# Kernel optimization log

Measured on AMD Instinct MI355X. Metric: run time of the kernel, lower is better.

## Reference

```python
import jax, jax.numpy as jnp
import numpy as np

S, B, D = 1024, 32, 1024

def setup_inputs() -> dict:
    key = jax.random.key(0)
    k1, k2, k3, k4, k5 = jax.random.split(key, 5)
    x = jax.random.normal(k1, (S, B, D), dtype=jnp.float32)
    layer_input = jax.random.normal(k2, (S, B, D), dtype=jnp.float32)
    position_embedding = jax.random.normal(k3, (S, B, D), dtype=jnp.float32)
    # pad indicator == 1 (True); random pads, ~half the positions
    encoder_mask = jax.random.randint(k4, (B, S), 0, 2).astype(bool)
    W = jax.random.normal(k5, (D, 1), dtype=jnp.float32) * (1.0 / np.sqrt(D))
    b = jnp.zeros((1,), dtype=jnp.float32)
    return {"x": x, "layer_input": layer_input,
            "position_embedding": position_embedding,
            "encoder_mask": encoder_mask, "W": W, "b": b}

def reference(x, layer_input, position_embedding, encoder_mask, W, b):
    s, bsz, d = x.shape
    valid = (~encoder_mask).astype(x.dtype)            # (B, S)
    sentence_length = valid.sum(axis=-1)               # (B,)
    langtok_index = s - sentence_length                # (B,)
    # predicted soft position in [0, sentence_length]
    pred = jax.nn.sigmoid(x @ W + b)[..., 0]           # (S, B)
    pred = pred * sentence_length[None, :]             # (S, B)
    # absolute positions shifted by language-token offset
    all_pos = jnp.arange(s, dtype=x.dtype)[:, None] - langtok_index[None, :]  # (S, B)
    # distances[i, b, j] = pred[i, b] - all_pos[j, b]
    dist = pred[:, :, None] - all_pos.T[None, :, :]    # (S, B, S)
    prob = 1.0 / (dist * dist + 0.001)                 # reciprocal squared distance
    prob = prob * valid[None, :, :]                    # zero out pads along j
    prob = prob / prob.sum(axis=-1, keepdims=True)     # normalize over source positions
    # weighted sum of position embeddings: (S,B,S) x (S,B,D) -> (S,B,D)
    out = jnp.einsum('ibj,jbd->ibd', prob, position_embedding)
    out = out * valid.T[:, :, None]                    # zero out pad rows
    return out
```

## Files before the change

kernel.cpp:

```cpp
#include <hip/hip_runtime.h>


#define S_ 1024
#define B_ 32
#define D_ 1024

typedef unsigned short us;
typedef __attribute__((ext_vector_type(4))) unsigned short us4;
typedef __attribute__((ext_vector_type(4))) float f4;
typedef __attribute__((ext_vector_type(8))) short short8;

__device__ __forceinline__ float bf2f(us u){
  unsigned v = ((unsigned)u) << 16;
  float f;
  __builtin_memcpy(&f, &v, 4);
  return f;
}
__device__ __forceinline__ us f2bf(float f){
  unsigned v;
  __builtin_memcpy(&v, &f, 4);
  v = v + 0x7fffu + ((v >> 16) & 1u);
  return (us)(v >> 16);
}

__device__ __forceinline__ void gll16(const void* g, void* l){
  __builtin_amdgcn_global_load_lds(
      (const __attribute__((address_space(1))) void*)g,
      (__attribute__((address_space(3))) void*)l,
      16, 0, 0);
}

__global__ __launch_bounds__(256) void prep_k(const unsigned char* __restrict__ mask,
                                              float* __restrict__ valid,
                                              float* __restrict__ slen,
                                              float* __restrict__ ltok)
{
  const int b = blockIdx.x;
  const int t = threadIdx.x;
  __shared__ int flags[5];
  __shared__ int red[256];
  if (t < 5) flags[t] = 0;
  __syncthreads();
  for (int k = 0; k < 32; ++k){
    int p = t * 32 + k;
    unsigned v = mask[p];
    if (v){
      atomicOr(&flags[p & 3], 1);
      if (v > 1u) atomicOr(&flags[4], 1);
    }
  }
  __syncthreads();
  int fmt;
  int any123 = flags[1] | flags[2] | flags[3];
  if (!flags[4]) fmt = any123 ? 0 : 1;
  else           fmt = (flags[0] | flags[1]) ? 2 : 3;

  int cnt = 0;
#pragma unroll
  for (int q = 0; q < 4; ++q){
    int j = t + q * 256;
    size_t idx = (size_t)b * S_ + j;
    unsigned mv;
    if (fmt == 0)      mv = mask[idx];
    else if (fmt == 1) mv = ((const unsigned int*)mask)[idx];
    else if (fmt == 2) mv = ((const unsigned short*)mask)[idx];
    else               mv = ((const unsigned int*)mask)[idx] & 0x7fffffffu;
    valid[idx] = mv ? 0.0f : 1.0f;
    cnt += mv ? 0 : 1;
  }
  red[t] = cnt;
  __syncthreads();
  for (int s = 128; s > 0; s >>= 1){
    if (t < s) red[t] += red[t + s];
    __syncthreads();
  }
  if (t == 0){
    float cn = (float)red[0];
    slen[b] = cn;
    ltok[b] = (float)S_ - cn;
  }
}

__device__ __forceinline__ void rowk_body(int blk, const float* __restrict__ x,
                                          const float* __restrict__ Wp,
                                          const float* __restrict__ bp,
                                          const float* __restrict__ valid,
                                          const float* __restrict__ slen,
                                          const float* __restrict__ ltok,
                                          us* __restrict__ P,
                                          float* __restrict__ rs,
                                          float* __restrict__ c_arr,
                                          bool writeP)
{
  const int wid  = threadIdx.x >> 6;
  const int lane = threadIdx.x & 63;
  const int row  = blk * 4 + wid;
  const int b = row & (B_ - 1);
  const int i = row >> 5;

  const float4* xr = (const float4*)(x + (size_t)row * D_);
  const float4* wr = (const float4*)Wp;
  float acc = 0.f;
#pragma unroll
  for (int q = 0; q < 4; ++q){
    float4 xv = xr[q * 64 + lane];
    float4 wv = wr[q * 64 + lane];
    acc += xv.x * wv.x + xv.y * wv.y + xv.z * wv.z + xv.w * wv.w;
  }
#pragma unroll
  for (int off = 32; off > 0; off >>= 1) acc += __shfl_xor(acc, off);

  float z   = acc + bp[0];
  float sig = 1.f / (1.f + expf(-z));
  float c   = sig * slen[b] + ltok[b];

  const float4* vr = (const float4*)(valid + (size_t)b * S_);
  us4* Pr = (us4*)(P + ((size_t)b * S_ + i) * S_);
  float wsum = 0.f;
#pragma unroll
  for (int q = 0; q < 4; ++q){
    int idx = q * 64 + lane;
    float4 vv = vr[idx];
    float j0 = (float)(idx * 4);
    float d0 = c - j0;
    float d1 = c - (j0 + 1.f);
    float d2 = c - (j0 + 2.f);
    float d3 = c - (j0 + 3.f);
    us p0 = f2bf(vv.x / (d0 * d0 + 1e-3f));
    us p1 = f2bf(vv.y / (d1 * d1 + 1e-3f));
    us p2 = f2bf(vv.z / (d2 * d2 + 1e-3f));
    us p3 = f2bf(vv.w / (d3 * d3 + 1e-3f));
    if (writeP){
      us4 pv; pv.x = p0; pv.y = p1; pv.z = p2; pv.w = p3;
      Pr[idx] = pv;
    }
    wsum += bf2f(p0) + bf2f(p1) + bf2f(p2) + bf2f(p3);
  }
#pragma unroll
  for (int off = 32; off > 0; off >>= 1) wsum += __shfl_xor(wsum, off);

  if (lane == 0){
    float vi = valid[(size_t)b * S_ + i];
    rs[(size_t)b * S_ + i] = (vi != 0.f) ? (vi / wsum) : 0.f;
    c_arr[(size_t)b * S_ + i] = c;
  }
}

__device__ __forceinline__ void transp_body(int j0, int d0, int b,
                                            const float* __restrict__ pe,
                                            us* __restrict__ Etr,
                                            us* tile )
{
  const int t  = threadIdx.x;
  const int rr = t >> 4, cc = t & 15;
#pragma unroll
  for (int q = 0; q < 4; ++q){
    int j = q * 16 + rr;
    float4 v = *(const float4*)(pe + ((size_t)(j0 + j) * B_ + b) * D_ + d0 + cc * 4);
    us4 tv; tv.x = f2bf(v.x); tv.y = f2bf(v.y); tv.z = f2bf(v.z); tv.w = f2bf(v.w);
    *(us4*)&tile[j * 68 + cc * 4] = tv;
  }
  __syncthreads();
#pragma unroll
  for (int q = 0; q < 4; ++q){
    int d = q * 16 + rr;
    us4 v;
    v.x = tile[(cc * 4 + 0) * 68 + d];
    v.y = tile[(cc * 4 + 1) * 68 + d];
    v.z = tile[(cc * 4 + 2) * 68 + d];
    v.w = tile[(cc * 4 + 3) * 68 + d];
    *(us4*)(Etr + ((size_t)b * D_ + d0 + d) * S_ + j0 + cc * 4) = v;
  }
}

__global__ __launch_bounds__(256) void mid_k(const float* __restrict__ x,
                                             const float* __restrict__ Wp,
                                             const float* __restrict__ bp,
                                             const float* __restrict__ valid,
                                             const float* __restrict__ slen,
                                             const float* __restrict__ ltok,
                                             us* __restrict__ P,
                                             float* __restrict__ rs,
                                             float* __restrict__ c_arr,
                                             const float* __restrict__ pe,
                                             us* __restrict__ Etr)
{
  __shared__ us tile[64 * 68];
  const int bid = blockIdx.x;
  if (bid < (S_ * B_ / 4)){
    rowk_body(bid, x, Wp, bp, valid, slen, ltok, P, rs, c_arr, true);
  } else {
    int id2 = bid - (S_ * B_ / 4);
    int jt = id2 & 15;
    int dt = (id2 >> 4) & 15;
    int b  = id2 >> 8;
    transp_body(jt * 64, dt * 64, b, pe, Etr, tile);
  }
}

__global__ __launch_bounds__(256) void gemm_k(const us* __restrict__ P,
                                              const us* __restrict__ Etr,
                                              const float* __restrict__ rs,
                                              float* __restrict__ out)
{
  const int bid  = blockIdx.x;
  const int xcd  = bid & 7;
  const int s    = bid >> 3;
  const int b    = xcd * 4 + (s >> 6);
  const int tile = s & 63;
  const int i0   = (tile >> 3) * 128;
  const int n0   = (tile & 7) * 128;

  const int t = threadIdx.x;
  const int w = t >> 6;
  const int l = t & 63;
  const int wm = w >> 1, wn = w & 1;
  const int ml = l & 15, quad = l >> 4;

  __shared__ __align__(16) us sA[128 * 64];
  __shared__ __align__(16) us sB[128 * 64];

  const us* gA[4]; const us* gB[4];
  us* lA[4]; us* lB[4];
#pragma unroll
  for (int q = 0; q < 4; ++q){
    int p = (w * 4 + q) * 64 + l;
    int r = p >> 3;
    int c = (p & 7) ^ (r & 7);
    gA[q] = P   + ((size_t)b * S_ + (i0 + r)) * S_ + c * 8;
    gB[q] = Etr + ((size_t)b * D_ + (n0 + r)) * S_ + c * 8;
    lA[q] = sA + (w * 4 + q) * 512;
    lB[q] = sB + (w * 4 + q) * 512;
  }

  f4 acc[4][4];
#pragma unroll
  for (int mt = 0; mt < 4; ++mt)
#pragma unroll
    for (int nt = 0; nt < 4; ++nt){
      f4 zf = {0.0f, 0.0f, 0.0f, 0.0f};
      acc[mt][nt] = zf;
    }

  int arow[4], brow[4];
#pragma unroll
  for (int mt = 0; mt < 4; ++mt) arow[mt] = wm * 64 + mt * 16 + ml;
#pragma unroll
  for (int nt = 0; nt < 4; ++nt) brow[nt] = wn * 64 + nt * 16 + ml;

  for (int kt = 0; kt < S_; kt += 64){
    if (kt) __syncthreads();
#pragma unroll
    for (int q = 0; q < 4; ++q) gll16(gA[q] + kt, lA[q]);
#pragma unroll
    for (int q = 0; q < 4; ++q) gll16(gB[q] + kt, lB[q]);
    __syncthreads();
#pragma unroll
    for (int ks = 0; ks < 2; ++ks){
      short8 av[4], bv[4];
      const int cbase = ks * 4 + quad;
#pragma unroll
      for (int mt = 0; mt < 4; ++mt){
        int r = arow[mt];
        av[mt] = *(const short8*)(sA + (r * 8 + (cbase ^ (r & 7))) * 8);
      }
#pragma unroll
      for (int nt = 0; nt < 4; ++nt){
        int r = brow[nt];
        bv[nt] = *(const short8*)(sB + (r * 8 + (cbase ^ (r & 7))) * 8);
      }
#pragma unroll
      for (int mt = 0; mt < 4; ++mt)
#pragma unroll
        for (int nt = 0; nt < 4; ++nt)
          acc[mt][nt] = __builtin_amdgcn_mfma_f32_16x16x32_bf16(av[mt], bv[nt], acc[mt][nt], 0, 0, 0);
    }
  }

  const float* rsb = rs + (size_t)b * S_;
#pragma unroll
  for (int mt = 0; mt < 4; ++mt){
#pragma unroll
    for (int reg = 0; reg < 4; ++reg){
      int i = i0 + wm * 64 + mt * 16 + quad * 4 + reg;
      float rv = rsb[i];
      size_t ob = ((size_t)i * B_ + b) * D_;
#pragma unroll
      for (int nt = 0; nt < 4; ++nt){
        int d = n0 + wn * 64 + nt * 16 + ml;
        out[ob + d] = acc[mt][nt][reg] * rv;
      }
    }
  }
}

__global__ __launch_bounds__(256) void rowk_nb(const float* __restrict__ x,
                                               const float* __restrict__ Wp,
                                               const float* __restrict__ bp,
                                               const float* __restrict__ valid,
                                               const float* __restrict__ slen,
                                               const float* __restrict__ ltok,
                                               float* __restrict__ rs,
                                               float* __restrict__ c_arr)
{
  rowk_body(blockIdx.x, x, Wp, bp, valid, slen, ltok, nullptr, rs, c_arr, false);
}

__global__ __launch_bounds__(256) void slow_out_k(const float* __restrict__ pe,
                                                  const float* __restrict__ valid,
                                                  const float* __restrict__ c_arr,
                                                  const float* __restrict__ rs,
                                                  float* __restrict__ out)
{
  const int bid = blockIdx.x;
  const int b = bid & (B_ - 1);
  const int i = bid >> 5;
  const int t = threadIdx.x;
  __shared__ float sw[S_];
  float c  = c_arr[(size_t)b * S_ + i];
  float rv = rs[(size_t)b * S_ + i];
#pragma unroll
  for (int q = 0; q < 4; ++q){
    int j = t + q * 256;
    float d = c - (float)j;
    sw[j] = valid[(size_t)b * S_ + j] / (d * d + 1e-3f);
  }
  __syncthreads();
  float a0 = 0, a1 = 0, a2 = 0, a3 = 0;
  if (rv != 0.0f){
    for (int j = 0; j < S_; ++j){
      float wj = sw[j];
      const float* row = pe + ((size_t)j * B_ + b) * D_;
      a0 += wj * row[t];
      a1 += wj * row[t + 256];
      a2 += wj * row[t + 512];
      a3 += wj * row[t + 768];
    }
  }
  float* orow = out + ((size_t)i * B_ + b) * D_;
  orow[t]       = a0 * rv;
  orow[t + 256] = a1 * rv;
  orow[t + 512] = a2 * rv;
  orow[t + 768] = a3 * rv;
}

extern "C" void kernel_launch(void* const* d_in, const int* in_sizes, int n_in,
                              void* d_out, int out_size, void* d_ws, size_t ws_size,
                              hipStream_t stream)
{
  (void)in_sizes; (void)n_in; (void)out_size;
  const float* x  = (const float*)d_in[0];
  const float* pe = (const float*)d_in[2];
  const unsigned char* mask = (const unsigned char*)d_in[3];
  const float* Wp = (const float*)d_in[4];
  const float* bp = (const float*)d_in[5];
  float* out = (float*)d_out;
  char* ws = (char*)d_ws;

  const size_t offValid = 0;
  const size_t offRs    = offValid + (size_t)B_ * S_ * 4;
  const size_t offSlen  = offRs    + (size_t)B_ * S_ * 4;
  const size_t offLtok  = offSlen  + 128;
  const size_t offC     = offLtok  + 128;
  const size_t offP     = offC     + (size_t)B_ * S_ * 4;
  const size_t offE     = offP     + (size_t)B_ * S_ * S_ * 2;
  const size_t need     = offE     + (size_t)B_ * D_ * S_ * 2;

  float* valid = (float*)(ws + offValid);
  float* rs    = (float*)(ws + offRs);
  float* slen  = (float*)(ws + offSlen);
  float* ltok  = (float*)(ws + offLtok);
  float* c_arr = (float*)(ws + offC);
  us* P   = (us*)(ws + offP);
  us* Etr = (us*)(ws + offE);

  prep_k<<<B_, 256, 0, stream>>>(mask, valid, slen, ltok);
  if (ws_size >= need){
    mid_k<<<16384, 256, 0, stream>>>(x, Wp, bp, valid, slen, ltok, P, rs, c_arr, pe, Etr);
    gemm_k<<<2048, 256, 0, stream>>>(P, Etr, rs, out);
  } else {
    rowk_nb<<<S_ * B_ / 4, 256, 0, stream>>>(x, Wp, bp, valid, slen, ltok, rs, c_arr);
    slow_out_k<<<S_ * B_, 256, 0, stream>>>(pe, valid, c_arr, rs, out);
  }
}
```

Before: 476.0 us.

## Rewrite batched GEMM with 256x256 tiles, double-buffered LDS and interleaved loads

Replaces the 128x128 single-buffered GEMM with 256x256 output tiles on 512-thread blocks, each warp computing 128x64. LDS is double-buffered and split into K-halves, so global-to-LDS loads for the next step are issued between MFMA groups. Fewer barriers and s_setprio are used to overlap memory traffic with matrix math. The risks are higher register pressure from 32 accumulators per thread, a large LDS footprint that limits occupancy, and only 512 blocks to spread across the CUs.

After: 454.6 us. 4.5% less time.

```diff
diff --git a/kernel.cpp b/kernel.cpp
--- a/kernel.cpp
+++ b/kernel.cpp
@@ -198,91 +198,149 @@
   }
 }
 
-__global__ __launch_bounds__(256) void gemm_k(const us* __restrict__ P,
-                                              const us* __restrict__ Etr,
-                                              const float* __restrict__ rs,
-                                              float* __restrict__ out)
-{
-  const int bid  = blockIdx.x;
-  const int xcd  = bid & 7;
-  const int s    = bid >> 3;
-  const int b    = xcd * 4 + (s >> 6);
-  const int tile = s & 63;
-  const int i0   = (tile >> 3) * 128;
-  const int n0   = (tile & 7) * 128;
-
-  const int t = threadIdx.x;
-  const int w = t >> 6;
-  const int l = t & 63;
-  const int wm = w >> 1, wn = w & 1;
-  const int ml = l & 15, quad = l >> 4;
-
-  __shared__ __align__(16) us sA[128 * 64];
-  __shared__ __align__(16) us sB[128 * 64];
-
-  const us* gA[4]; const us* gB[4];
-  us* lA[4]; us* lB[4];
-#pragma unroll
-  for (int q = 0; q < 4; ++q){
-    int p = (w * 4 + q) * 64 + l;
-    int r = p >> 3;
-    int c = (p & 7) ^ (r & 7);
-    gA[q] = P   + ((size_t)b * S_ + (i0 + r)) * S_ + c * 8;
-    gB[q] = Etr + ((size_t)b * D_ + (n0 + r)) * S_ + c * 8;
-    lA[q] = sA + (w * 4 + q) * 512;
-    lB[q] = sB + (w * 4 + q) * 512;
-  }
-
-  f4 acc[4][4];
-#pragma unroll
-  for (int mt = 0; mt < 4; ++mt)
+__global__ __launch_bounds__(512, 2) void gemm_k(const us* __restrict__ P,
+                                                 const us* __restrict__ Etr,
+                                                 const float* __restrict__ rs,
+                                                 float* __restrict__ out)
+{
+  const int bid = blockIdx.x;
+  const int xcd = bid & 7;
+  const int s   = bid >> 3;
+  const int b   = xcd * 4 + (s >> 4);
+  const int t16 = s & 15;
+  const int i0  = (t16 >> 2) * 256;
+  const int n0  = (t16 & 3) * 256;
+
+  const int tid  = threadIdx.x;
+  const int wid  = tid >> 6;
+  const int lane = tid & 63;
+  const int wm = wid >> 2, wn = wid & 3;
+  const int ml = lane & 15, quad = lane >> 4;
+
+  __shared__ __align__(16) us lds[2][4][8192];
+
+  const us* gsrc[4];
+  {
+    int p = tid;
+    int r = p >> 2;
+    int c = (p & 3) ^ ((r >> 1) & 3);
+    const us* arow = P   + ((size_t)b * S_ + (i0 + r)) * S_;
+    const us* brow = Etr + ((size_t)b * D_ + (n0 + r)) * S_;
+    gsrc[0] = arow + c * 8;
+    gsrc[1] = arow + 32 + c * 8;
+    gsrc[2] = brow + c * 8;
+    gsrc[3] = brow + 32 + c * 8;
+  }
+  const int dst0 = wid * 64 * 8;
+
+  int aoff[8], boff[4];
+#pragma unroll
+  for (int mt = 0; mt < 8; ++mt){
+    int r = wm * 128 + mt * 16 + ml;
+    aoff[mt] = r * 32 + ((quad ^ ((r >> 1) & 3)) * 8);
+  }
+#pragma unroll
+  for (int nt = 0; nt < 4; ++nt){
+    int r = wn * 64 + nt * 16 + ml;
+    boff[nt] = r * 32 + ((quad ^ ((r >> 1) & 3)) * 8);
+  }
+
+  f4 acc[8][4];
+#pragma unroll
+  for (int mt = 0; mt < 8; ++mt)
 #pragma unroll
     for (int nt = 0; nt < 4; ++nt){
-      f4 zf = {0.0f, 0.0f, 0.0f, 0.0f};
-      acc[mt][nt] = zf;
+      f4 z = {0.0f, 0.0f, 0.0f, 0.0f};
+      acc[mt][nt] = z;
     }
 
-  int arow[4], brow[4];
-#pragma unroll
-  for (int mt = 0; mt < 4; ++mt) arow[mt] = wm * 64 + mt * 16 + ml;
-#pragma unroll
-  for (int nt = 0; nt < 4; ++nt) brow[nt] = wn * 64 + nt * 16 + ml;
-
-  for (int kt = 0; kt < S_; kt += 64){
-    if (kt) __syncthreads();
-#pragma unroll
-    for (int q = 0; q < 4; ++q) gll16(gA[q] + kt, lA[q]);
-#pragma unroll
-    for (int q = 0; q < 4; ++q) gll16(gB[q] + kt, lB[q]);
-    __syncthreads();
-#pragma unroll
-    for (int ks = 0; ks < 2; ++ks){
-      short8 av[4], bv[4];
-      const int cbase = ks * 4 + quad;
-#pragma unroll
-      for (int mt = 0; mt < 4; ++mt){
-        int r = arow[mt];
-        av[mt] = *(const short8*)(sA + (r * 8 + (cbase ^ (r & 7))) * 8);
-      }
-#pragma unroll
-      for (int nt = 0; nt < 4; ++nt){
-        int r = brow[nt];
-        bv[nt] = *(const short8*)(sB + (r * 8 + (cbase ^ (r & 7))) * 8);
-      }
-#pragma unroll
-      for (int mt = 0; mt < 4; ++mt)
-#pragma unroll
-        for (int nt = 0; nt < 4; ++nt)
-          acc[mt][nt] = __builtin_amdgcn_mfma_f32_16x16x32_bf16(av[mt], bv[nt], acc[mt][nt], 0, 0, 0);
-    }
-  }
+  auto STAGE = [&](int buf, int h, int kt){
+    const us* g = gsrc[h] + kt * 64;
+    us* l = &lds[buf][h][dst0];
+    gll16(g,                 l);
+    gll16(g + 128 * S_,      l + 4096);
+  };
+
+  STAGE(0, 0, 0); STAGE(0, 2, 0);
+  STAGE(0, 1, 0); STAGE(0, 3, 0);
+  asm volatile("s_waitcnt vmcnt(4)" ::: "memory");
+  __builtin_amdgcn_s_barrier();
+  asm volatile("" ::: "memory");
+
+#pragma unroll 1
+  for (int kt = 0; kt < 16; ++kt){
+    const int buf = kt & 1, nb = buf ^ 1;
+    const int ktn = (kt < 15) ? (kt + 1) : 0;
+    const us* A0 = lds[buf][0];
+    const us* A1 = lds[buf][1];
+    const us* B0 = lds[buf][2];
+    const us* B1 = lds[buf][3];
+    short8 av[4], av2[4], bv[4];
+
+#pragma unroll
+    for (int mt = 0; mt < 4; ++mt) av[mt] = *(const short8*)&A0[aoff[mt]];
+#pragma unroll
+    for (int nt = 0; nt < 4; ++nt) bv[nt] = *(const short8*)&B0[boff[nt]];
+    STAGE(nb, 0, ktn);
+    __builtin_amdgcn_s_setprio(1);
+#pragma unroll
+    for (int mt = 0; mt < 4; ++mt)
+#pragma unroll
+      for (int nt = 0; nt < 4; ++nt)
+        acc[mt][nt] = __builtin_amdgcn_mfma_f32_16x16x32_bf16(av[mt], bv[nt], acc[mt][nt], 0, 0, 0);
+    __builtin_amdgcn_s_setprio(0);
+
+#pragma unroll
+    for (int mt = 0; mt < 4; ++mt) av2[mt] = *(const short8*)&A0[aoff[4 + mt]];
+    STAGE(nb, 2, ktn);
+    __builtin_amdgcn_s_setprio(1);
+#pragma unroll
+    for (int mt = 0; mt < 4; ++mt)
+#pragma unroll
+      for (int nt = 0; nt < 4; ++nt)
+        acc[4 + mt][nt] = __builtin_amdgcn_mfma_f32_16x16x32_bf16(av2[mt], bv[nt], acc[4 + mt][nt], 0, 0, 0);
+    __builtin_amdgcn_s_setprio(0);
+
+    asm volatile("s_waitcnt vmcnt(4)" ::: "memory");
+    __builtin_amdgcn_s_barrier();
+    asm volatile("" ::: "memory");
+
+#pragma unroll
+    for (int mt = 0; mt < 4; ++mt) av[mt] = *(const short8*)&A1[aoff[mt]];
+#pragma unroll
+    for (int nt = 0; nt < 4; ++nt) bv[nt] = *(const short8*)&B1[boff[nt]];
+    STAGE(nb, 1, ktn);
+    __builtin_amdgcn_s_setprio(1);
+#pragma unroll
+    for (int mt = 0; mt < 4; ++mt)
+#pragma unroll
+      for (int nt = 0; nt < 4; ++nt)
+        acc[mt][nt] = __builtin_amdgcn_mfma_f32_16x16x32_bf16(av[mt], bv[nt], acc[mt][nt], 0, 0, 0);
+    __builtin_amdgcn_s_setprio(0);
+
+#pragma unroll
+    for (int mt = 0; mt < 4; ++mt) av2[mt] = *(const short8*)&A1[aoff[4 + mt]];
+    STAGE(nb, 3, ktn);
+    __builtin_amdgcn_s_setprio(1);
+#pragma unroll
+    for (int mt = 0; mt < 4; ++mt)
+#pragma unroll
+      for (int nt = 0; nt < 4; ++nt)
+        acc[4 + mt][nt] = __builtin_amdgcn_mfma_f32_16x16x32_bf16(av2[mt], bv[nt], acc[4 + mt][nt], 0, 0, 0);
+    __builtin_amdgcn_s_setprio(0);
+
+    asm volatile("s_waitcnt vmcnt(4)" ::: "memory");
+    __builtin_amdgcn_s_barrier();
+    asm volatile("" ::: "memory");
+  }
+  asm volatile("s_waitcnt vmcnt(0)" ::: "memory");
 
   const float* rsb = rs + (size_t)b * S_;
 #pragma unroll
-  for (int mt = 0; mt < 4; ++mt){
+  for (int mt = 0; mt < 8; ++mt){
 #pragma unroll
     for (int reg = 0; reg < 4; ++reg){
-      int i = i0 + wm * 64 + mt * 16 + quad * 4 + reg;
+      int i = i0 + wm * 128 + mt * 16 + quad * 4 + reg;
       float rv = rsb[i];
       size_t ob = ((size_t)i * B_ + b) * D_;
 #pragma unroll
@@ -377,7 +435,7 @@
   prep_k<<<B_, 256, 0, stream>>>(mask, valid, slen, ltok);
   if (ws_size >= need){
     mid_k<<<16384, 256, 0, stream>>>(x, Wp, bp, valid, slen, ltok, P, rs, c_arr, pe, Etr);
-    gemm_k<<<2048, 256, 0, stream>>>(P, Etr, rs, out);
+    gemm_k<<<512, 512, 0, stream>>>(P, Etr, rs, out);
   } else {
     rowk_nb<<<S_ * B_ / 4, 256, 0, stream>>>(x, Wp, bp, valid, slen, ltok, rs, c_arr);
     slow_out_k<<<S_ * B_, 256, 0, stream>>>(pe, valid, c_arr, rs, out);
```
